# Kernel optimization log

Hardware: AMD Instinct MI355X
Metric: run time of the kernel (lower is better)

## Reference

```python
import jax, jax.numpy as jnp
import numpy as np

B, H, L, D = 8, 16, 1024, 64

def setup_inputs() -> dict:
    key = jax.random.key(0)
    kq, kk, kv = jax.random.split(key, 3)
    q = jax.random.normal(kq, (B, H, L, D), dtype=jnp.float32)
    k = jax.random.normal(kk, (B, H, L, D), dtype=jnp.float32)
    v = jax.random.normal(kv, (B, H, L, D), dtype=jnp.float32)
    # causal mask, broadcast over batch and head
    mask = jnp.tril(jnp.ones((L, L), dtype=jnp.int32))[None, None, :, :]
    return {"q": q, "k": k, "v": v, "mask": mask}

def reference(q, k, v, mask):
    b, h, l, d = q.shape
    # FAITHFUL to original: k.view(b, h, d, l) is a reshape, NOT a transpose
    k_t = k.reshape(b, h, d, l)
    score = jnp.matmul(q, k_t) / np.sqrt(d).astype(np.float32)  # [b,h,l,l]
    # FAITHFUL to original bug: masked_fill(mask==0, -e) with e=1e-12
    score = jnp.where(mask == 0, jnp.float32(-1e-12), score)
    attn = jax.nn.softmax(score, axis=-1)
    out = jnp.matmul(attn, v)  # [b,h,l,d]
    return (out, attn)
```

## Files before the change

### kernel.cpp

```cpp
#include <hip/hip_runtime.h>

#define L_  1024
#define D_  64
#define TM  128
#define TN  64
#define LDK 72
#define NT  (L_ / TN)

typedef __attribute__((ext_vector_type(8))) short          short8;
typedef __attribute__((ext_vector_type(8))) unsigned short ushort8;
typedef __attribute__((ext_vector_type(4))) float          f32x4;

__device__ __forceinline__ unsigned short bf16r(float f) {
    unsigned u = __builtin_bit_cast(unsigned, f);
    u += 0x7fffu + ((u >> 16) & 1u);
    return (unsigned short)(u >> 16);
}

__global__ __launch_bounds__(256, 2)
void sdpa_kernel(const float* __restrict__ q, const float* __restrict__ kmat,
                 const float* __restrict__ v, float* __restrict__ out,
                 float* __restrict__ attn)
{
    __shared__ __align__(16) unsigned short Qs[TM * LDK];
    __shared__ __align__(16) unsigned short Ks[TN * LDK];
    __shared__ __align__(16) unsigned short Vs[D_ * LDK];
    __shared__ __align__(16) unsigned short Ps[TM * LDK];

    const int t    = threadIdx.x;
    const int wave = t >> 6;
    const int lane = t & 63;
    const int quad = lane >> 4;
    const int l15  = lane & 15;
    const int bh   = blockIdx.x;
    const int rt   = blockIdx.y;
    const int m0   = rt * TM;
    const int rowA = wave * 32;

    const float* qb = q    + (size_t)bh * (L_ * D_);
    const float* kb = kmat + (size_t)bh * (L_ * D_);
    const float* vb = v    + (size_t)bh * (L_ * D_);
    float* outb  = out  + (size_t)bh * (L_ * D_);
    float* attnb = attn + (size_t)bh * ((size_t)L_ * L_);

    #pragma unroll
    for (int i = 0; i < 8; ++i) {
        int idx = (i * 256 + t) * 4;
        int m = idx >> 6, c = idx & 63;
        float4 f = *(const float4*)&qb[(size_t)(m0 + m) * D_ + c];
        ushort4 b;
        b.x = bf16r(f.x); b.y = bf16r(f.y); b.z = bf16r(f.z); b.w = bf16r(f.w);
        *(ushort4*)&Qs[m * LDK + c] = b;
    }

    auto stageK = [&](int nt) {
        const int ng = t & 31, kg = t >> 5;
        const float* src = kb + (size_t)(kg * 8) * L_ + nt * TN + 2 * ng;
        float2 a[8];
        #pragma unroll
        for (int j = 0; j < 8; ++j) a[j] = *(const float2*)(src + (size_t)j * L_);
        ushort8 r0, r1;
        #pragma unroll
        for (int j = 0; j < 8; ++j) { r0[j] = bf16r(a[j].x); r1[j] = bf16r(a[j].y); }
        *(ushort8*)&Ks[(2 * ng)     * LDK + kg * 8] = r0;
        *(ushort8*)&Ks[(2 * ng + 1) * LDK + kg * 8] = r1;
    };
    auto stageV = [&](int nt) {
        const int cg = t & 31, ngp = t >> 5;
        const float* src = vb + (size_t)(nt * TN + ngp * 8) * D_ + 2 * cg;
        float2 a[8];
        #pragma unroll
        for (int j = 0; j < 8; ++j) a[j] = *(const float2*)(src + (size_t)j * D_);
        ushort8 r0, r1;
        #pragma unroll
        for (int j = 0; j < 8; ++j) { r0[j] = bf16r(a[j].x); r1[j] = bf16r(a[j].y); }
        *(ushort8*)&Vs[(2 * cg)     * LDK + ngp * 8] = r0;
        *(ushort8*)&Vs[(2 * cg + 1) * LDK + ngp * 8] = r1;
    };

    auto computeScoreT = [&](f32x4 (&acc)[2][4]) {
        #pragma unroll
        for (int ks = 0; ks < 2; ++ks) {
            const int cu = ks * 32 + quad * 8;
            short8 af[2];
            #pragma unroll
            for (int tr = 0; tr < 2; ++tr)
                af[tr] = *(const short8*)&Qs[(rowA + tr * 16 + l15) * LDK + cu];
            #pragma unroll
            for (int tc = 0; tc < 4; ++tc) {
                short8 bfr = *(const short8*)&Ks[(tc * 16 + l15) * LDK + cu];
                #pragma unroll
                for (int tr = 0; tr < 2; ++tr)
                    acc[tr][tc] = __builtin_amdgcn_mfma_f32_16x16x32_bf16(bfr, af[tr], acc[tr][tc], 0, 0, 0);
            }
        }
    };

    const f32x4 zero4 = {0.f, 0.f, 0.f, 0.f};

    float zpart[2][4] = {};
    const int ntmax1 = (m0 + TM - 1) / TN;
    __syncthreads();
    for (int nt = 0; nt <= ntmax1; ++nt) {
        stageK(nt);
        __syncthreads();
        f32x4 acc[2][4];
        #pragma unroll
        for (int tr = 0; tr < 2; ++tr)
            #pragma unroll
            for (int tc = 0; tc < 4; ++tc) acc[tr][tc] = zero4;
        computeScoreT(acc);
        #pragma unroll
        for (int tr = 0; tr < 2; ++tr) {
            const int gm = m0 + rowA + tr * 16 + l15;
            #pragma unroll
            for (int tc = 0; tc < 4; ++tc)
                #pragma unroll
                for (int r = 0; r < 4; ++r) {
                    const int gn = nt * TN + tc * 16 + quad * 4 + r;
                    zpart[tr][tc] += (gn > gm) ? 1.0f : __expf(acc[tr][tc][r] * 0.125f);
                }
        }
        __syncthreads();
    }
    const float zmissing = (float)(L_ - (ntmax1 + 1) * TN);
    float rcpz[2];
    #pragma unroll
    for (int tr = 0; tr < 2; ++tr) {
        float z = (zpart[tr][0] + zpart[tr][1]) + (zpart[tr][2] + zpart[tr][3]);
        z += __shfl_xor(z, 16);
        z += __shfl_xor(z, 32);
        rcpz[tr] = 1.0f / (z + zmissing);
    }

    f32x4 oacc[2][4];
    #pragma unroll
    for (int tr = 0; tr < 2; ++tr)
        #pragma unroll
        for (int tc = 0; tc < 4; ++tc) oacc[tr][tc] = zero4;

    for (int nt = 0; nt < NT; ++nt) {
        const bool fullmask = (nt * TN) > (m0 + TM - 1);
        __syncthreads();
        if (!fullmask) stageK(nt);
        stageV(nt);
        __syncthreads();

        if (!fullmask) {
            f32x4 acc[2][4];
            #pragma unroll
            for (int tr = 0; tr < 2; ++tr)
                #pragma unroll
                for (int tc = 0; tc < 4; ++tc) acc[tr][tc] = zero4;
            computeScoreT(acc);
            #pragma unroll
            for (int tr = 0; tr < 2; ++tr) {
                const int lrow = rowA + tr * 16 + l15;
                const int gm = m0 + lrow;
                const float rz = rcpz[tr];
                #pragma unroll
                for (int tc = 0; tc < 4; ++tc) {
                    float p[4];
                    #pragma unroll
                    for (int r = 0; r < 4; ++r) {
                        const int gn = nt * TN + tc * 16 + quad * 4 + r;
                        float e = (gn > gm) ? 1.0f : __expf(acc[tr][tc][r] * 0.125f);
                        p[r] = e * rz;
                    }
                    float4 vv = {p[0], p[1], p[2], p[3]};
                    *(float4*)&attnb[(size_t)gm * L_ + nt * TN + tc * 16 + quad * 4] = vv;
                    ushort4 pw;
                    pw.x = bf16r(p[0]); pw.y = bf16r(p[1]);
                    pw.z = bf16r(p[2]); pw.w = bf16r(p[3]);
                    *(ushort4*)&Ps[lrow * LDK + tc * 16 + quad * 4] = pw;
                }
            }
        } else {
            const bool firstFull = (nt == ntmax1 + 1);
            #pragma unroll
            for (int tr = 0; tr < 2; ++tr) {
                const int lrow = rowA + tr * 16 + l15;
                const int gm = m0 + lrow;
                const float rz = rcpz[tr];
                float4 vv = {rz, rz, rz, rz};
                const unsigned short pb = bf16r(rz);
                ushort4 p4; p4.x = pb; p4.y = pb; p4.z = pb; p4.w = pb;
                #pragma unroll
                for (int c = 0; c < 4; ++c) {
                    *(float4*)&attnb[(size_t)gm * L_ + nt * TN + c * 16 + quad * 4] = vv;
                    if (firstFull)
                        *(ushort4*)&Ps[lrow * LDK + c * 16 + quad * 4] = p4;
                }
            }
        }
        __syncthreads();

        #pragma unroll
        for (int ks = 0; ks < 2; ++ks) {
            const int cu = ks * 32 + quad * 8;
            short8 pf[2];
            #pragma unroll
            for (int tr = 0; tr < 2; ++tr)
                pf[tr] = *(const short8*)&Ps[(rowA + tr * 16 + l15) * LDK + cu];
            #pragma unroll
            for (int tc = 0; tc < 4; ++tc) {
                short8 vf = *(const short8*)&Vs[(tc * 16 + l15) * LDK + cu];
                #pragma unroll
                for (int tr = 0; tr < 2; ++tr)
                    oacc[tr][tc] = __builtin_amdgcn_mfma_f32_16x16x32_bf16(pf[tr], vf, oacc[tr][tc], 0, 0, 0);
            }
        }
    }

    #pragma unroll
    for (int tr = 0; tr < 2; ++tr)
        #pragma unroll
        for (int r = 0; r < 4; ++r) {
            const int gm = m0 + rowA + tr * 16 + quad * 4 + r;
            #pragma unroll
            for (int tc = 0; tc < 4; ++tc)
                outb[(size_t)gm * D_ + tc * 16 + l15] = oacc[tr][tc][r];
        }
}

extern "C" void kernel_launch(void* const* d_in, const int* in_sizes, int n_in,
                              void* d_out, int out_size, void* d_ws, size_t ws_size,
                              hipStream_t stream) {
    (void)in_sizes; (void)n_in; (void)d_ws; (void)ws_size; (void)out_size;
    const float* q = (const float*)d_in[0];
    const float* k = (const float*)d_in[1];
    const float* v = (const float*)d_in[2];
    float* out  = (float*)d_out;
    float* attn = (float*)d_out + (size_t)8 * 16 * 1024 * 64;
    dim3 grid(128, 8);
    sdpa_kernel<<<grid, dim3(256), 0, stream>>>(q, k, v, out, attn);
}
```

Baseline: 716.5 us.

## Double-buffer K/V tiles in LDS with register prefetch of next tile

```diff
diff --git a/kernel.cpp b/kernel.cpp
--- a/kernel.cpp
+++ b/kernel.cpp
@@ -23,8 +23,8 @@
                  float* __restrict__ attn)
 {
     __shared__ __align__(16) unsigned short Qs[TM * LDK];
-    __shared__ __align__(16) unsigned short Ks[TN * LDK];
-    __shared__ __align__(16) unsigned short Vs[D_ * LDK];
+    __shared__ __align__(16) unsigned short Ks[2][TN * LDK];
+    __shared__ __align__(16) unsigned short Vs[2][D_ * LDK];
     __shared__ __align__(16) unsigned short Ps[TM * LDK];
 
     const int t    = threadIdx.x;
@@ -53,32 +53,35 @@
         *(ushort4*)&Qs[m * LDK + c] = b;
     }
 
-    auto stageK = [&](int nt) {
-        const int ng = t & 31, kg = t >> 5;
+    const int ng = t & 31, kg = t >> 5;
+    float2 rK[8], rV[8];
+
+    auto loadK = [&](int nt) {
         const float* src = kb + (size_t)(kg * 8) * L_ + nt * TN + 2 * ng;
-        float2 a[8];
-        #pragma unroll
-        for (int j = 0; j < 8; ++j) a[j] = *(const float2*)(src + (size_t)j * L_);
+        #pragma unroll
+        for (int j = 0; j < 8; ++j) rK[j] = *(const float2*)(src + (size_t)j * L_);
+    };
+    auto writeK = [&](unsigned short* dst) {
         ushort8 r0, r1;
         #pragma unroll
-        for (int j = 0; j < 8; ++j) { r0[j] = bf16r(a[j].x); r1[j] = bf16r(a[j].y); }
-        *(ushort8*)&Ks[(2 * ng)     * LDK + kg * 8] = r0;
-        *(ushort8*)&Ks[(2 * ng + 1) * LDK + kg * 8] = r1;
-    };
-    auto stageV = [&](int nt) {
-        const int cg = t & 31, ngp = t >> 5;
-        const float* src = vb + (size_t)(nt * TN + ngp * 8) * D_ + 2 * cg;
-        float2 a[8];
-        #pragma unroll
-        for (int j = 0; j < 8; ++j) a[j] = *(const float2*)(src + (size_t)j * D_);
+        for (int j = 0; j < 8; ++j) { r0[j] = bf16r(rK[j].x); r1[j] = bf16r(rK[j].y); }
+        *(ushort8*)&dst[(2 * ng)     * LDK + kg * 8] = r0;
+        *(ushort8*)&dst[(2 * ng + 1) * LDK + kg * 8] = r1;
+    };
+    auto loadV = [&](int nt) {
+        const float* src = vb + (size_t)(nt * TN + kg * 8) * D_ + 2 * ng;
+        #pragma unroll
+        for (int j = 0; j < 8; ++j) rV[j] = *(const float2*)(src + (size_t)j * D_);
+    };
+    auto writeV = [&](unsigned short* dst) {
         ushort8 r0, r1;
         #pragma unroll
-        for (int j = 0; j < 8; ++j) { r0[j] = bf16r(a[j].x); r1[j] = bf16r(a[j].y); }
-        *(ushort8*)&Vs[(2 * cg)     * LDK + ngp * 8] = r0;
-        *(ushort8*)&Vs[(2 * cg + 1) * LDK + ngp * 8] = r1;
-    };
-
-    auto computeScoreT = [&](f32x4 (&acc)[2][4]) {
+        for (int j = 0; j < 8; ++j) { r0[j] = bf16r(rV[j].x); r1[j] = bf16r(rV[j].y); }
+        *(ushort8*)&dst[(2 * ng)     * LDK + kg * 8] = r0;
+        *(ushort8*)&dst[(2 * ng + 1) * LDK + kg * 8] = r1;
+    };
+
+    auto computeScoreT = [&](f32x4 (&acc)[2][4], const unsigned short* ksrc) {
         #pragma unroll
         for (int ks = 0; ks < 2; ++ks) {
             const int cu = ks * 32 + quad * 8;
@@ -88,7 +91,7 @@
                 af[tr] = *(const short8*)&Qs[(rowA + tr * 16 + l15) * LDK + cu];
             #pragma unroll
             for (int tc = 0; tc < 4; ++tc) {
-                short8 bfr = *(const short8*)&Ks[(tc * 16 + l15) * LDK + cu];
+                short8 bfr = *(const short8*)&ksrc[(tc * 16 + l15) * LDK + cu];
                 #pragma unroll
                 for (int tr = 0; tr < 2; ++tr)
                     acc[tr][tc] = __builtin_amdgcn_mfma_f32_16x16x32_bf16(bfr, af[tr], acc[tr][tc], 0, 0, 0);
@@ -100,16 +103,16 @@
 
     float zpart[2][4] = {};
     const int ntmax1 = (m0 + TM - 1) / TN;
-    __syncthreads();
+    loadK(0); writeK(Ks[0]);
     for (int nt = 0; nt <= ntmax1; ++nt) {
-        stageK(nt);
         __syncthreads();
+        if (nt < ntmax1) loadK(nt + 1);
         f32x4 acc[2][4];
         #pragma unroll
         for (int tr = 0; tr < 2; ++tr)
             #pragma unroll
             for (int tc = 0; tc < 4; ++tc) acc[tr][tc] = zero4;
-        computeScoreT(acc);
+        computeScoreT(acc, Ks[nt & 1]);
         #pragma unroll
         for (int tr = 0; tr < 2; ++tr) {
             const int gm = m0 + rowA + tr * 16 + l15;
@@ -121,9 +124,11 @@
                     zpart[tr][tc] += (gn > gm) ? 1.0f : __expf(acc[tr][tc][r] * 0.125f);
                 }
         }
-        __syncthreads();
+        if (nt < ntmax1) writeK(Ks[(nt + 1) & 1]);
     }
     const float zmissing = (float)(L_ - (ntmax1 + 1) * TN);
+
+    loadK(0); loadV(0);
     float rcpz[2];
     #pragma unroll
     for (int tr = 0; tr < 2; ++tr) {
@@ -132,6 +137,8 @@
         z += __shfl_xor(z, 32);
         rcpz[tr] = 1.0f / (z + zmissing);
     }
+    __syncthreads();
+    writeK(Ks[0]); writeV(Vs[0]);
 
     f32x4 oacc[2][4];
     #pragma unroll
@@ -142,9 +149,11 @@
     for (int nt = 0; nt < NT; ++nt) {
         const bool fullmask = (nt * TN) > (m0 + TM - 1);
         __syncthreads();
-        if (!fullmask) stageK(nt);
-        stageV(nt);
-        __syncthreads();
+        const int nn = nt + 1;
+        const bool nextV = (nn < NT);
+        const bool nextK = nextV && ((nn * TN) <= (m0 + TM - 1));
+        if (nextV) loadV(nn);
+        if (nextK) loadK(nn);
 
         if (!fullmask) {
             f32x4 acc[2][4];
@@ -152,7 +161,7 @@
             for (int tr = 0; tr < 2; ++tr)
                 #pragma unroll
                 for (int tc = 0; tc < 4; ++tc) acc[tr][tc] = zero4;
-            computeScoreT(acc);
+            computeScoreT(acc, Ks[nt & 1]);
             #pragma unroll
             for (int tr = 0; tr < 2; ++tr) {
                 const int lrow = rowA + tr * 16 + l15;
@@ -193,7 +202,6 @@
                 }
             }
         }
-        __syncthreads();
 
         #pragma unroll
         for (int ks = 0; ks < 2; ++ks) {
@@ -204,12 +212,15 @@
                 pf[tr] = *(const short8*)&Ps[(rowA + tr * 16 + l15) * LDK + cu];
             #pragma unroll
             for (int tc = 0; tc < 4; ++tc) {
-                short8 vf = *(const short8*)&Vs[(tc * 16 + l15) * LDK + cu];
+                short8 vf = *(const short8*)&Vs[nt & 1][(tc * 16 + l15) * LDK + cu];
                 #pragma unroll
                 for (int tr = 0; tr < 2; ++tr)
                     oacc[tr][tc] = __builtin_amdgcn_mfma_f32_16x16x32_bf16(pf[tr], vf, oacc[tr][tc], 0, 0, 0);
             }
         }
+
+        if (nextV) writeV(Vs[nn & 1]);
+        if (nextK) writeK(Ks[nn & 1]);
     }
 
     #pragma unroll
```

Result: no change. 714.9 us (-0.2%).
